# Kernel tuning notes

Measured on AMD Instinct MI355X. Metric: run time of the kernel, lower is better.

## Reference

```python
import jax, jax.numpy as jnp
import numpy as np

B, K, D, NH = 4096, 32, 1024, 16
HD = D // NH
LN_EPS = 1e-5
RMS_EPS = 1e-6


def layernorm(x, g, b):
    mu = jnp.mean(x, axis=-1, keepdims=True)
    var = jnp.mean((x - mu) ** 2, axis=-1, keepdims=True)
    return (x - mu) * jax.lax.rsqrt(var + LN_EPS) * g + b


def rmsnorm(x, g):
    ms = jnp.mean(x ** 2, axis=-1, keepdims=True)
    return x * jax.lax.rsqrt(ms + RMS_EPS) * g


def setup_inputs() -> dict:
    key = jax.random.key(0)
    ks = jax.random.split(key, 12)
    s = 0.02
    inp = {
        "query": jax.random.normal(ks[0], (B, D), jnp.float32),
        "point_features": jax.random.normal(ks[1], (B, K, D), jnp.float32),
        "lnq_g": jnp.ones((D,), jnp.float32),
        "lnq_b": jnp.zeros((D,), jnp.float32),
        "lnkv_g": jnp.ones((D,), jnp.float32),
        "lnkv_b": jnp.zeros((D,), jnp.float32),
        "Wq": jax.random.normal(ks[2], (D, D), jnp.float32) * s,
        "bq": jnp.zeros((D,), jnp.float32),
        "Wk": jax.random.normal(ks[3], (D, D), jnp.float32) * s,
        "bk": jnp.zeros((D,), jnp.float32),
        "Wv": jax.random.normal(ks[4], (D, D), jnp.float32) * s,
        "bv": jnp.zeros((D,), jnp.float32),
        "rmsq_g": jnp.ones((D,), jnp.float32),
        "rmsk_g": jnp.ones((D,), jnp.float32),
        "Wo": jax.random.normal(ks[5], (D, D), jnp.float32) * s,
        "bo": jnp.zeros((D,), jnp.float32),
        "mlpn_g": jnp.ones((D,), jnp.float32),
        "mlpn_b": jnp.zeros((D,), jnp.float32),
        "W1": jax.random.normal(ks[6], (D, 4 * D), jnp.float32) * s,
        "b1": jnp.zeros((4 * D,), jnp.float32),
        "W2": jax.random.normal(ks[7], (4 * D, D), jnp.float32) * s,
        "b2": jnp.zeros((D,), jnp.float32),
    }
    return inp


def reference(query, point_features, lnq_g, lnq_b, lnkv_g, lnkv_b,
              Wq, bq, Wk, bk, Wv, bv, rmsq_g, rmsk_g, Wo, bo,
              mlpn_g, mlpn_b, W1, b1, W2, b2):
    q_in = layernorm(query, lnq_g, lnq_b)            # [B, D]
    kv_in = layernorm(point_features, lnkv_g, lnkv_b)  # [B, K, D]

    q = rmsnorm(q_in @ Wq + bq, rmsq_g)              # [B, D]
    k = rmsnorm(kv_in @ Wk + bk, rmsk_g)             # [B, K, D]
    v = kv_in @ Wv + bv                               # [B, K, D]

    # Faithful to original: raw row-major reshape [B,K,D] -> [B,NH,K,HD]
    qh = q.reshape(B, NH, HD)                         # [B, NH, HD] (q_len = 1)
    kh = k.reshape(B, NH, K, HD)
    vh = v.reshape(B, NH, K, HD)

    scores = jnp.einsum('bhd,bhkd->bhk', qh, kh) / np.sqrt(HD).astype(np.float32)
    attn = jax.nn.softmax(scores, axis=-1)            # [B, NH, K]
    out = jnp.einsum('bhk,bhkd->bhd', attn, vh)       # [B, NH, HD]

    # Faithful: transpose(1,2) then reshape -> [B, HD, NH] -> [B, D]
    out = jnp.transpose(out, (0, 2, 1)).reshape(B, D)
    out = (out @ Wo + bo) + query                     # residual

    h = layernorm(out, mlpn_g, mlpn_b)
    mlp_out = (jax.nn.gelu(h @ W1 + b1, approximate=False) @ W2) + b2
    return out + mlp_out
```

## Files before the change

kernel.cpp:

```cpp
#include <hip/hip_runtime.h>
#include <stdint.h>

#define DEVI __device__ __forceinline__

typedef unsigned short u16;
typedef short s8v __attribute__((ext_vector_type(8)));
typedef float f4v __attribute__((ext_vector_type(4)));
typedef u16 u16x4 __attribute__((ext_vector_type(4)));

DEVI u16 f2bf(float f) {
  unsigned u = __float_as_uint(f);
  u += 0x7fffu + ((u >> 16) & 1u);
  return (u16)(u >> 16);
}
DEVI float bf2f(u16 h) { return __uint_as_float(((unsigned)h) << 16); }

DEVI void gload16(const void* g, void* l) {
  __builtin_amdgcn_global_load_lds(
      (const __attribute__((address_space(1))) void*)(uintptr_t)g,
      (__attribute__((address_space(3))) void*)(uintptr_t)l, 16, 0, 0);
}

__global__ __launch_bounds__(256) void transpose_w(const float* __restrict__ W,
                                                   u16* __restrict__ Wt, int R, int C) {
  __shared__ float tile[32][33];
  const int tx = threadIdx.x & 31, ty = threadIdx.x >> 5;
  const int r0 = blockIdx.y * 32, c0 = blockIdx.x * 32;
#pragma unroll
  for (int i = 0; i < 4; ++i)
    tile[ty + 8 * i][tx] = W[(size_t)(r0 + ty + 8 * i) * C + c0 + tx];
  __syncthreads();
#pragma unroll
  for (int i = 0; i < 4; ++i)
    Wt[(size_t)(c0 + ty + 8 * i) * R + r0 + tx] = f2bf(tile[tx][ty + 8 * i]);
}

__global__ __launch_bounds__(256) void ln_rows(const float* __restrict__ x,
                                               const float* __restrict__ g,
                                               const float* __restrict__ bsh,
                                               u16* __restrict__ y,
                                               float* __restrict__ zbuf) {
  const size_t row = blockIdx.x;
  const int t = threadIdx.x;
  if (zbuf && t == 0) zbuf[row] = 0.f;
  float4 v = ((const float4*)(x + row * 1024))[t];
  float s = v.x + v.y + v.z + v.w;
  float q = v.x * v.x + v.y * v.y + v.z * v.z + v.w * v.w;
#pragma unroll
  for (int m = 1; m < 64; m <<= 1) { s += __shfl_xor(s, m); q += __shfl_xor(q, m); }
  __shared__ float sh[8];
  if ((t & 63) == 0) { sh[t >> 6] = s; sh[4 + (t >> 6)] = q; }
  __syncthreads();
  s = sh[0] + sh[1] + sh[2] + sh[3];
  q = sh[4] + sh[5] + sh[6] + sh[7];
  const float mu = s * (1.f / 1024.f);
  const float var = q * (1.f / 1024.f) - mu * mu;
  const float rs = rsqrtf(var + 1e-5f);
  const int c = t * 4;
  const float in[4] = {v.x, v.y, v.z, v.w};
  u16x4 o;
#pragma unroll
  for (int i = 0; i < 4; ++i) o[i] = f2bf((in[i] - mu) * rs * g[c + i] + bsh[c + i]);
  *(u16x4*)(y + row * 1024 + c) = o;
}

template <int EPI>
__global__ __launch_bounds__(512, 2) void gemm256(
    const u16* __restrict__ A, const u16* __restrict__ Bt,
    const float* __restrict__ biasK, const float* __restrict__ biasV,
    const float* __restrict__ gcol, u16* __restrict__ CK, u16* __restrict__ CV,
    float* __restrict__ rowssq, int M, int N, int K, int RB, int CB) {
  __shared__ u16 lds[4][16384];
  const int t = threadIdx.x;
  const int lane = t & 63;
  const int wave = t >> 6;
  const int wm = wave >> 2, wn = wave & 3;
  const int fr = lane & 15, kq = lane >> 4;

  const int bid = blockIdx.x;
  const int cpx = gridDim.x >> 3;
  const int swz = (bid & 7) * cpx + (bid >> 3);
  const int rb = swz / CB, cb = swz % CB;
  const size_t row0 = (size_t)rb * 256, col0 = (size_t)cb * 256;

  f4v acc[8][4];
#pragma unroll
  for (int i = 0; i < 8; ++i)
#pragma unroll
    for (int n = 0; n < 4; ++n) acc[i][n] = (f4v){0.f, 0.f, 0.f, 0.f};

  const int srow = t >> 2;
  const int scol = (((t & 3) ^ ((t >> 3) & 3)) << 3);
  const u16* Ag0 = A + (row0 + srow) * (size_t)K + scol;
  const u16* Ag1 = Ag0 + (size_t)128 * K;
  const u16* Bg0 = Bt + (col0 + srow) * (size_t)K + scol;
  const u16* Bg1 = Bg0 + (size_t)128 * K;

  const int kx = ((kq ^ ((fr >> 1) & 3)) << 3);

  const int NT = K >> 5;

#pragma unroll
  for (int tt = 0; tt < 3; ++tt) {
    u16* sA = &lds[tt][0];
    u16* sB = &lds[tt][8192];
    gload16(Ag0 + tt * 32, sA + t * 8);
    gload16(Ag1 + tt * 32, sA + 4096 + t * 8);
    gload16(Bg0 + tt * 32, sB + t * 8);
    gload16(Bg1 + tt * 32, sB + 4096 + t * 8);
  }

#pragma unroll 4
  for (int T = 0; T < NT; ++T) {
    asm volatile("s_waitcnt vmcnt(8)" ::: "memory");
    __builtin_amdgcn_s_barrier();
    __builtin_amdgcn_sched_barrier(0);
    const u16* sA = &lds[T & 3][0];
    const u16* sB = &lds[T & 3][8192];
    const int Ts = (T + 3 < NT) ? T + 3 : NT - 1;
    u16* dA = &lds[(T + 3) & 3][0];
    u16* dB = &lds[(T + 3) & 3][8192];
    s8v a[4], b[4];
#pragma unroll
    for (int m = 0; m < 4; ++m)
      a[m] = *(const s8v*)&sA[(wm * 128 + m * 16 + fr) * 32 + kx];
#pragma unroll
    for (int n = 0; n < 4; ++n)
      b[n] = *(const s8v*)&sB[(wn * 64 + n * 16 + fr) * 32 + kx];
    gload16(Ag0 + Ts * 32, dA + t * 8);
    gload16(Ag1 + Ts * 32, dA + 4096 + t * 8);
    __builtin_amdgcn_s_barrier();
    asm volatile("s_waitcnt lgkmcnt(0)" ::: "memory");
    __builtin_amdgcn_sched_barrier(0);
    __builtin_amdgcn_s_setprio(1);
#pragma unroll
    for (int m = 0; m < 4; ++m)
#pragma unroll
      for (int n = 0; n < 4; ++n)
        acc[m][n] = __builtin_amdgcn_mfma_f32_16x16x32_bf16(a[m], b[n], acc[m][n], 0, 0, 0);
    __builtin_amdgcn_s_setprio(0);
    __builtin_amdgcn_s_barrier();
#pragma unroll
    for (int m = 0; m < 4; ++m)
      a[m] = *(const s8v*)&sA[(wm * 128 + 64 + m * 16 + fr) * 32 + kx];
    gload16(Bg0 + Ts * 32, dB + t * 8);
    gload16(Bg1 + Ts * 32, dB + 4096 + t * 8);
    __builtin_amdgcn_s_barrier();
    asm volatile("s_waitcnt lgkmcnt(0)" ::: "memory");
    __builtin_amdgcn_sched_barrier(0);
    __builtin_amdgcn_s_setprio(1);
#pragma unroll
    for (int m = 0; m < 4; ++m)
#pragma unroll
      for (int n = 0; n < 4; ++n)
        acc[4 + m][n] = __builtin_amdgcn_mfma_f32_16x16x32_bf16(a[m], b[n], acc[4 + m][n], 0, 0, 0);
    __builtin_amdgcn_s_setprio(0);
  }

  const int kq4 = kq * 4;
  if (EPI == 0) {
    const bool isK = (col0 < 1024);
    if (isK) {
#pragma unroll
      for (int ai = 0; ai < 8; ++ai) {
        int cols[4];
        float bb[4], gg[4];
#pragma unroll
        for (int n = 0; n < 4; ++n) {
          cols[n] = (int)col0 + wn * 64 + n * 16 + fr;
          bb[n] = biasK[cols[n]];
          gg[n] = gcol[cols[n]];
        }
#pragma unroll
        for (int r = 0; r < 4; ++r) {
          const size_t grow = row0 + wm * 128 + ai * 16 + kq4 + r;
          float v[4];
#pragma unroll
          for (int n = 0; n < 4; ++n) v[n] = acc[ai][n][r] + bb[n];
          float s = v[0] * v[0] + v[1] * v[1] + v[2] * v[2] + v[3] * v[3];
          s += __shfl_xor(s, 1);
          s += __shfl_xor(s, 2);
          s += __shfl_xor(s, 4);
          s += __shfl_xor(s, 8);
          if (fr == 0) atomicAdd(&rowssq[grow], s);
#pragma unroll
          for (int n = 0; n < 4; ++n)
            CK[grow * 1024 + cols[n]] = f2bf(v[n] * gg[n]);
        }
      }
    } else {
#pragma unroll
      for (int ai = 0; ai < 8; ++ai) {
        int cols[4];
        float bb[4];
#pragma unroll
        for (int n = 0; n < 4; ++n) {
          cols[n] = (int)col0 - 1024 + wn * 64 + n * 16 + fr;
          bb[n] = biasV[cols[n]];
        }
#pragma unroll
        for (int r = 0; r < 4; ++r) {
          const size_t grow = row0 + wm * 128 + ai * 16 + kq4 + r;
#pragma unroll
          for (int n = 0; n < 4; ++n)
            CV[grow * 1024 + cols[n]] = f2bf(acc[ai][n][r] + bb[n]);
        }
      }
    }
  } else {
#pragma unroll
    for (int ai = 0; ai < 8; ++ai) {
      int cols[4];
      float bb[4];
#pragma unroll
      for (int n = 0; n < 4; ++n) {
        cols[n] = (int)col0 + wn * 64 + n * 16 + fr;
        bb[n] = biasK[cols[n]];
      }
#pragma unroll
      for (int r = 0; r < 4; ++r) {
        const size_t grow = row0 + wm * 128 + ai * 16 + kq4 + r;
#pragma unroll
        for (int n = 0; n < 4; ++n) {
          const float x = acc[ai][n][r] + bb[n];
          CK[grow * (size_t)N + cols[n]] = f2bf(0.5f * x * (1.f + erff(x * 0.70710678118654752f)));
        }
      }
    }
  }
}

template <int EPI>
__global__ __launch_bounds__(256) void gemm_bt(
    const u16* __restrict__ A, const u16* __restrict__ Bt,
    const float* __restrict__ bias, const float* __restrict__ gcol,
    void* __restrict__ Cv, const float* __restrict__ extra,
    float* __restrict__ rowssq, int M, int N, int K) {
  __shared__ u16 As[128 * 32];
  __shared__ u16 Bs[128 * 32];
  const int t = threadIdx.x;
  const int lane = t & 63;
  const int wave = t >> 6;
  const int wr = wave >> 1, wc = wave & 1;
  const size_t row0 = (size_t)blockIdx.y * 128;
  const size_t col0 = (size_t)blockIdx.x * 128;
  int Ksub = K, koff = 0;
  if (EPI == 6) { Ksub = K / gridDim.z; koff = blockIdx.z * Ksub; }

  f4v acc[4][4];
#pragma unroll
  for (int m = 0; m < 4; ++m)
#pragma unroll
    for (int n = 0; n < 4; ++n) acc[m][n] = (f4v){0.f, 0.f, 0.f, 0.f};

  const int sr = t >> 2;
  const int scw = (((t & 3) ^ ((t >> 3) & 3)) << 3);
  const u16* Ag = A + (row0 + sr) * (size_t)K + koff + scw;
  const u16* Bg = Bt + (col0 + sr) * (size_t)K + koff + scw;
  u16* Al = &As[t * 8];
  u16* Bl = &Bs[t * 8];
  const int fr = lane & 15;
  const int kx = (((lane >> 4) ^ ((fr >> 1) & 3)) << 3);

  for (int k0 = 0; k0 < Ksub; k0 += 32) {
    gload16(Ag + k0, Al);
    gload16(Ag + k0 + (size_t)64 * K, Al + 64 * 32);
    gload16(Bg + k0, Bl);
    gload16(Bg + k0 + (size_t)64 * K, Bl + 64 * 32);
    __syncthreads();
    s8v a[4], b[4];
#pragma unroll
    for (int m = 0; m < 4; ++m)
      a[m] = *(const s8v*)&As[(wr * 64 + m * 16 + fr) * 32 + kx];
#pragma unroll
    for (int n = 0; n < 4; ++n)
      b[n] = *(const s8v*)&Bs[(wc * 64 + n * 16 + fr) * 32 + kx];
#pragma unroll
    for (int m = 0; m < 4; ++m)
#pragma unroll
      for (int n = 0; n < 4; ++n)
        acc[m][n] = __builtin_amdgcn_mfma_f32_16x16x32_bf16(a[m], b[n], acc[m][n], 0, 0, 0);
    __syncthreads();
  }

  float* Cp = (float*)Cv;
  if (EPI == 6) Cp += (size_t)blockIdx.z * M * (size_t)N;
  const int rg = (lane >> 4) * 4;
#pragma unroll
  for (int m = 0; m < 4; ++m) {
    int cols[4];
    float bvals[4];
#pragma unroll
    for (int n = 0; n < 4; ++n) {
      cols[n] = (int)col0 + wc * 64 + n * 16 + fr;
      bvals[n] = (EPI == 6) ? 0.f : bias[cols[n]];
    }
#pragma unroll
    for (int r = 0; r < 4; ++r) {
      const size_t grow = row0 + wr * 64 + m * 16 + rg + r;
      float v[4];
#pragma unroll
      for (int n = 0; n < 4; ++n) v[n] = acc[m][n][r] + bvals[n];
      if (EPI == 5) {
        float s = v[0] * v[0] + v[1] * v[1] + v[2] * v[2] + v[3] * v[3];
        s += __shfl_xor(s, 1);
        s += __shfl_xor(s, 2);
        s += __shfl_xor(s, 4);
        s += __shfl_xor(s, 8);
        if (fr == 0) atomicAdd(&rowssq[grow], s);
      }
#pragma unroll
      for (int n = 0; n < 4; ++n) {
        const size_t idx = grow * (size_t)N + cols[n];
        if (EPI == 3) {
          Cp[idx] = v[n] + extra[idx];
        } else if (EPI == 5) {
          ((u16*)Cv)[idx] = f2bf(v[n]);
        } else if (EPI == 6) {
          Cp[idx] = v[n];
        }
      }
    }
  }
}

__global__ __launch_bounds__(256) void attn_k(const u16* __restrict__ qf,
                                              const u16* __restrict__ kmat,
                                              const float* __restrict__ kssq,
                                              const u16* __restrict__ vmat,
                                              const float* __restrict__ gq,
                                              const float* __restrict__ qssq,
                                              u16* __restrict__ ao) {
  const int lb = blockIdx.x;
  const int t = threadIdx.x;
  const int wave = t >> 6, lane = t & 63;
  const int j = lane & 31, half = lane >> 5;
  const float rq = rsqrtf(qssq[lb] * (1.f / 1024.f) + 1e-6f) * 0.125f;
  __shared__ float po[64][17];
#pragma unroll
  for (int hi = 0; hi < 4; ++hi) {
    const int h = wave * 4 + hi;
    const int krow = lb * 32 + 2 * h + (j >> 4);
    const u16* kp = kmat + (size_t)krow * 1024 + (j & 15) * 64 + half * 32;
    const u16* qp = qf + (size_t)lb * 1024 + h * 64 + half * 32;
    const float* gqp = gq + h * 64 + half * 32;
    float s = 0.f;
#pragma unroll
    for (int cc = 0; cc < 4; ++cc) {
      s8v qv = *(const s8v*)(qp + cc * 8);
      s8v kv = *(const s8v*)(kp + cc * 8);
#pragma unroll
      for (int e = 0; e < 8; ++e)
        s += bf2f((u16)qv[e]) * gqp[cc * 8 + e] * bf2f((u16)kv[e]);
    }
    s += __shfl_xor(s, 32);
    s *= rsqrtf(kssq[krow] * (1.f / 1024.f) + 1e-6f) * rq;
    float mx = s;
#pragma unroll
    for (int m = 16; m >= 1; m >>= 1) mx = fmaxf(mx, __shfl_xor(mx, m));
    const float pe = __expf(s - mx);
    float sum = pe;
#pragma unroll
    for (int m = 16; m >= 1; m >>= 1) sum += __shfl_xor(sum, m);
    const float pr = pe / sum;
    float o = 0.f;
#pragma unroll
    for (int jj = 0; jj < 32; ++jj) {
      const int vrow = lb * 32 + 2 * h + (jj >> 4);
      const float vv = bf2f(vmat[(size_t)vrow * 1024 + (jj & 15) * 64 + lane]);
      o += __shfl(pr, jj) * vv;
    }
    po[lane][h] = o;
  }
  __syncthreads();
  const int c = t * 4;
  u16x4 o4;
#pragma unroll
  for (int i = 0; i < 4; ++i) o4[i] = f2bf(po[(c + i) >> 4][(c + i) & 15]);
  *(u16x4*)(ao + (size_t)lb * 1024 + c) = o4;
}

__global__ __launch_bounds__(256) void combine_k(const float* __restrict__ p0,
                                                 const float* __restrict__ p1,
                                                 const float* __restrict__ b2,
                                                 const float* __restrict__ resid,
                                                 float* __restrict__ out) {
  const int i = blockIdx.x * 256 + threadIdx.x;
  float4 a = ((const float4*)p0)[i];
  float4 b = ((const float4*)p1)[i];
  float4 r = ((const float4*)resid)[i];
  float4 bb = ((const float4*)b2)[i & 255];
  float4 o;
  o.x = a.x + b.x + r.x + bb.x;
  o.y = a.y + b.y + r.y + bb.y;
  o.z = a.z + b.z + r.z + bb.z;
  o.w = a.w + b.w + r.w + bb.w;
  ((float4*)out)[i] = o;
}

extern "C" void kernel_launch(void* const* d_in, const int* in_sizes, int n_in,
                              void* d_out, int out_size, void* d_ws, size_t ws_size,
                              hipStream_t stream) {
  const float* query  = (const float*)d_in[0];
  const float* pf     = (const float*)d_in[1];
  const float* lnq_g  = (const float*)d_in[2];
  const float* lnq_b  = (const float*)d_in[3];
  const float* lnkv_g = (const float*)d_in[4];
  const float* lnkv_b = (const float*)d_in[5];
  const float* Wq     = (const float*)d_in[6];
  const float* bq     = (const float*)d_in[7];
  const float* Wk     = (const float*)d_in[8];
  const float* bk     = (const float*)d_in[9];
  const float* Wv     = (const float*)d_in[10];
  const float* bv     = (const float*)d_in[11];
  const float* rmsq_g = (const float*)d_in[12];
  const float* rmsk_g = (const float*)d_in[13];
  const float* Wo     = (const float*)d_in[14];
  const float* bo     = (const float*)d_in[15];
  const float* mlpn_g = (const float*)d_in[16];
  const float* mlpn_b = (const float*)d_in[17];
  const float* W1     = (const float*)d_in[18];
  const float* b1     = (const float*)d_in[19];
  const float* W2     = (const float*)d_in[20];
  const float* b2     = (const float*)d_in[21];
  float* out = (float*)d_out;

  char* p = (char*)d_ws;
  auto alloc = [&](size_t n) {
    char* r = p;
    p += (n + 255) & ~(size_t)255;
    return r;
  };

  u16* Wqt = (u16*)alloc((size_t)1024 * 1024 * 2);
  u16* KVt = (u16*)alloc((size_t)2048 * 1024 * 2);
  u16* Wot = (u16*)alloc((size_t)1024 * 1024 * 2);
  u16* W1t = (u16*)alloc((size_t)1024 * 4096 * 2);
  u16* W2t = (u16*)alloc((size_t)4096 * 1024 * 2);
  u16* qln = (u16*)alloc((size_t)4096 * 1024 * 2);
  u16* qpre = (u16*)alloc((size_t)4096 * 1024 * 2);
  float* qssq = (float*)alloc((size_t)4096 * 4);
  u16* attn_o = (u16*)alloc((size_t)4096 * 1024 * 2);
  float* outbuf = (float*)alloc((size_t)4096 * 1024 * 4);
  u16* hbuf = (u16*)alloc((size_t)4096 * 1024 * 2);
  u16* mid = (u16*)alloc((size_t)4096 * 4096 * 2);
  float* w2p = (float*)alloc((size_t)2 * 4096 * 1024 * 4);
  const size_t ROWS = 131072;
  u16* kvln = (u16*)alloc(ROWS * 2048);
  u16* kmat = (u16*)alloc(ROWS * 2048);
  u16* vmat = (u16*)alloc(ROWS * 2048);
  float* kssq = (float*)alloc(ROWS * 4);

  transpose_w<<<dim3(32, 32), 256, 0, stream>>>(Wq, Wqt, 1024, 1024);
  transpose_w<<<dim3(32, 32), 256, 0, stream>>>(Wk, KVt, 1024, 1024);
  transpose_w<<<dim3(32, 32), 256, 0, stream>>>(Wv, KVt + (size_t)1024 * 1024, 1024, 1024);
  transpose_w<<<dim3(32, 32), 256, 0, stream>>>(Wo, Wot, 1024, 1024);
  transpose_w<<<dim3(128, 32), 256, 0, stream>>>(W1, W1t, 1024, 4096);
  transpose_w<<<dim3(32, 128), 256, 0, stream>>>(W2, W2t, 4096, 1024);

  ln_rows<<<4096, 256, 0, stream>>>(query, lnq_g, lnq_b, qln, qssq);
  gemm_bt<5><<<dim3(8, 32), 256, 0, stream>>>(qln, Wqt, bq, nullptr, qpre, nullptr,
                                              qssq, 4096, 1024, 1024);

  ln_rows<<<(unsigned)ROWS, 256, 0, stream>>>(pf, lnkv_g, lnkv_b, kvln, kssq);
  gemm256<0><<<512 * 8, 512, 0, stream>>>(kvln, KVt, bk, bv, rmsk_g, kmat, vmat,
                                          kssq, (int)ROWS, 2048, 1024, 512, 8);
  attn_k<<<4096, 256, 0, stream>>>(qpre, kmat, kssq, vmat, rmsq_g, qssq, attn_o);

  gemm_bt<3><<<dim3(8, 32), 256, 0, stream>>>(attn_o, Wot, bo, nullptr, outbuf, query,
                                              nullptr, 4096, 1024, 1024);
  ln_rows<<<4096, 256, 0, stream>>>(outbuf, mlpn_g, mlpn_b, hbuf, nullptr);
  gemm256<1><<<16 * 16, 512, 0, stream>>>(hbuf, W1t, b1, nullptr, nullptr, mid, nullptr,
                                          nullptr, 4096, 4096, 1024, 16, 16);
  gemm_bt<6><<<dim3(8, 32, 2), 256, 0, stream>>>(mid, W2t, nullptr, nullptr, w2p,
                                                 nullptr, nullptr, 4096, 1024, 4096);
  combine_k<<<4096, 256, 0, stream>>>(w2p, w2p + (size_t)4096 * 1024, b2, outbuf, out);
}
```

Measured before the change: 1.093 ms.

## Chunk KV layernorm, projection and attention over batch slices to shrink buffers

Splits the 131072-row KV pipeline (layernorm, K/V projection GEMM, attention) into NC batch chunks, with NC chosen as the smallest power of two from 4 that fits the workspace. The intermediate kvln, kmat and vmat buffers then hold only one chunk. This lets them fit in the workspace and may let them stay in the large last-level cache between the producing and consuming kernels, cutting HBM traffic. The cost is more kernel launches and smaller grids per launch, which can lower occupancy and add launch-boundary tail effects.

```diff
diff --git a/kernel.cpp b/kernel.cpp
--- a/kernel.cpp
+++ b/kernel.cpp
@@ -445,11 +445,19 @@
   u16* hbuf = (u16*)alloc((size_t)4096 * 1024 * 2);
   u16* mid = (u16*)alloc((size_t)4096 * 4096 * 2);
   float* w2p = (float*)alloc((size_t)2 * 4096 * 1024 * 4);
-  const size_t ROWS = 131072;
-  u16* kvln = (u16*)alloc(ROWS * 2048);
-  u16* kmat = (u16*)alloc(ROWS * 2048);
-  u16* vmat = (u16*)alloc(ROWS * 2048);
-  float* kssq = (float*)alloc(ROWS * 4);
+
+  const size_t used = (size_t)(p - (char*)d_ws);
+  int NC = 4;
+  while (NC < 64) {
+    size_t rows_try = (size_t)131072 / NC;
+    if (used + 3 * (rows_try * 2048 + 256) + rows_try * 4 + 256 <= ws_size) break;
+    NC *= 2;
+  }
+  const size_t rows = (size_t)131072 / NC;
+  u16* kvln = (u16*)alloc(rows * 2048);
+  u16* kmat = (u16*)alloc(rows * 2048);
+  u16* vmat = (u16*)alloc(rows * 2048);
+  float* kssq = (float*)alloc(rows * 4);
 
   transpose_w<<<dim3(32, 32), 256, 0, stream>>>(Wq, Wqt, 1024, 1024);
   transpose_w<<<dim3(32, 32), 256, 0, stream>>>(Wk, KVt, 1024, 1024);
@@ -462,10 +470,17 @@
   gemm_bt<5><<<dim3(8, 32), 256, 0, stream>>>(qln, Wqt, bq, nullptr, qpre, nullptr,
                                               qssq, 4096, 1024, 1024);
 
-  ln_rows<<<(unsigned)ROWS, 256, 0, stream>>>(pf, lnkv_g, lnkv_b, kvln, kssq);
-  gemm256<0><<<512 * 8, 512, 0, stream>>>(kvln, KVt, bk, bv, rmsk_g, kmat, vmat,
-                                          kssq, (int)ROWS, 2048, 1024, 512, 8);
-  attn_k<<<4096, 256, 0, stream>>>(qpre, kmat, kssq, vmat, rmsq_g, qssq, attn_o);
+  const int bpc = 4096 / NC;
+  const int RB = (int)(rows / 256);
+  for (int c = 0; c < NC; ++c) {
+    ln_rows<<<(unsigned)rows, 256, 0, stream>>>(pf + (size_t)c * rows * 1024, lnkv_g,
+                                                lnkv_b, kvln, kssq);
+    gemm256<0><<<RB * 8, 512, 0, stream>>>(kvln, KVt, bk, bv, rmsk_g, kmat, vmat,
+                                           kssq, (int)rows, 2048, 1024, RB, 8);
+    attn_k<<<bpc, 256, 0, stream>>>(qpre + (size_t)c * bpc * 1024, kmat, kssq, vmat,
+                                    rmsq_g, qssq + (size_t)c * bpc,
+                                    attn_o + (size_t)c * bpc * 1024);
+  }
 
   gemm_bt<3><<<dim3(8, 32), 256, 0, stream>>>(attn_o, Wot, bo, nullptr, outbuf, query,
                                               nullptr, 4096, 1024, 1024);
```

Result: no change. 1.079 ms (-1.2%).
